# Kernel optimization log

Measured on AMD Instinct MI355X. Metric: run time of the kernel, lower is better.

The kernel has to match this reference:

```python
import jax, jax.numpy as jnp
import numpy as np

B, T, I, U = 64, 1024, 512, 1024


def ternary_quantize(w):
    # alpha = mean|w|; threshold = 0.7*alpha; map to {-alpha, 0, alpha}
    alpha = jnp.mean(jnp.abs(w))
    thr = 0.7 * alpha
    w_t = jnp.where(jnp.abs(w) < thr, jnp.zeros_like(w), jnp.sign(w))
    return alpha * w_t


def setup_inputs() -> dict:
    key = jax.random.key(0)
    k1, k2, k3 = jax.random.split(key, 3)
    x = jax.random.normal(k1, (B, T, I), dtype=jnp.float32)
    kernel = jax.random.normal(k2, (I, 4 * U), dtype=jnp.float32) * 0.05
    recurrent_kernel = jax.random.normal(k3, (U, 4 * U), dtype=jnp.float32) * 0.05
    # keras unit_forget_bias: zeros except ones on the forget-gate quarter
    bias = jnp.concatenate([jnp.zeros((U,)), jnp.ones((U,)), jnp.zeros((2 * U,))]).astype(jnp.float32)
    return {"x": x, "kernel": kernel, "recurrent_kernel": recurrent_kernel, "bias": bias}


def reference(x, kernel, recurrent_kernel, bias):
    kq = ternary_quantize(kernel)            # [I, 4U]
    rq = ternary_quantize(recurrent_kernel)  # [U, 4U]
    # Precompute input projection for all timesteps (math identical to per-step matmul)
    xz = jnp.einsum('bti,ig->btg', x, kq) + bias  # [B, T, 4U]
    xz_t = jnp.transpose(xz, (1, 0, 2))           # [T, B, 4U]

    def step(carry, zx):
        h, c = carry
        z = zx + h @ rq                            # [B, 4U]
        zi, zf, zg, zo = jnp.split(z, 4, axis=-1)  # keras gate order i, f, c, o
        i = jax.nn.sigmoid(zi)
        f = jax.nn.sigmoid(zf)
        g = jnp.tanh(zg)
        o = jax.nn.sigmoid(zo)
        c_new = f * c + i * g
        h_new = o * jnp.tanh(c_new)
        return (h_new, c_new), h_new

    h0 = jnp.zeros((x.shape[0], U), dtype=x.dtype)
    c0 = jnp.zeros((x.shape[0], U), dtype=x.dtype)
    _, hs = jax.lax.scan(step, (h0, c0), xz_t)     # hs: [T, B, U]
    return jnp.transpose(hs, (1, 0, 2))            # return_sequences=True -> [B, T, U]
```

## Files before the change

kernel.cpp:

```cpp
#include <hip/hip_runtime.h>
#include <hip/hip_bf16.h>


typedef __attribute__((ext_vector_type(8))) __bf16 bf16x8;
typedef __attribute__((ext_vector_type(4))) float f32x4;
typedef __attribute__((ext_vector_type(2))) unsigned int u32x2;

#define NWG 256
#define WGT 512
#define T_N 1024

__global__ void absum_kernel(const float* __restrict__ w, int n,
                             double* __restrict__ partial) {
  __shared__ double sd[256];
  double s = 0.0;
  for (int i = blockIdx.x * 256 + threadIdx.x; i < n; i += 256 * 256)
    s += fabs((double)w[i]);
  sd[threadIdx.x] = s;
  __syncthreads();
  for (int k = 128; k > 0; k >>= 1) {
    if (threadIdx.x < k) sd[threadIdx.x] += sd[threadIdx.x + k];
    __syncthreads();
  }
  if (threadIdx.x == 0) partial[blockIdx.x] = sd[0];
}

__global__ void alpha_finalize(const double* __restrict__ pk,
                               const double* __restrict__ pr,
                               float* __restrict__ alphas) {
  __shared__ double sd[256];
  int t = threadIdx.x;
  sd[t] = pk[t];
  __syncthreads();
  for (int s = 128; s > 0; s >>= 1) {
    if (t < s) sd[t] += sd[t + s];
    __syncthreads();
  }
  if (t == 0) alphas[0] = (float)(sd[0] / (512.0 * 4096.0));
  __syncthreads();
  sd[t] = pr[t];
  __syncthreads();
  for (int s = 128; s > 0; s >>= 1) {
    if (t < s) sd[t] += sd[t + s];
    __syncthreads();
  }
  if (t == 0) alphas[1] = (float)(sd[0] / (1024.0 * 4096.0));
}

__global__ void quant_kernel(const float* __restrict__ w, int kbits,
                             const float* __restrict__ alphas, int ai,
                             __hip_bfloat16* __restrict__ wt, int total) {
  int idx = blockIdx.x * 256 + threadIdx.x;
  if (idx >= total) return;
  float thr = 0.7f * alphas[ai];
  int K = 1 << kbits;
  int c = idx >> kbits;
  int k = idx & (K - 1);
  float v = w[k * 4096 + (c & 3) * 1024 + (c >> 2)];
  float q = (fabsf(v) < thr) ? 0.0f : ((v > 0.0f) ? 1.0f : ((v < 0.0f) ? -1.0f : 0.0f));
  wt[idx] = __float2bfloat16(q);
}

__device__ __forceinline__ bf16x8 cvt2(f32x4 a, f32x4 b) {
  bf16x8 r;
  r[0] = (__bf16)a[0]; r[1] = (__bf16)a[1];
  r[2] = (__bf16)a[2]; r[3] = (__bf16)a[3];
  r[4] = (__bf16)b[0]; r[5] = (__bf16)b[1];
  r[6] = (__bf16)b[2]; r[7] = (__bf16)b[3];
  return r;
}
__device__ __forceinline__ void ld16cc(bf16x8* d, const __hip_bfloat16* p) {
  asm volatile("global_load_dwordx4 %0, %1, off sc0 sc1"
               : "=v"(*d) : "v"(p) : "memory");
}
__device__ __forceinline__ void st8cc(__hip_bfloat16* p, u32x2 v) {
  asm volatile("global_store_dwordx2 %0, %1, off sc0 sc1" ::"v"(p), "v"(v)
               : "memory");
}
__device__ __forceinline__ void stflag(int* p, int v) {
  asm volatile("global_store_dword %0, %1, off sc0 sc1" ::"v"(p), "v"(v)
               : "memory");
}
__device__ __forceinline__ int ldflag(const int* p) {
  int v;
  asm volatile("global_load_dword %0, %1, off sc0 sc1\n\ts_waitcnt vmcnt(0)"
               : "=v"(v) : "v"(p) : "memory");
  return v;
}
__device__ __forceinline__ unsigned bf16b(float f) {
  return (unsigned)__builtin_bit_cast(unsigned short, __float2bfloat16(f));
}
__device__ __forceinline__ float sigm(float z) { return 1.0f / (1.0f + __expf(-z)); }
__device__ __forceinline__ float tanhx(float z) {
  float e = __expf(-2.0f * fabsf(z));
  return __builtin_copysignf((1.0f - e) / (1.0f + e), z);
}

__device__ __forceinline__ void wg_wait(const int* fl, int tgt, int* lflag,
                                        int lane, int wave) {
  if (wave == 7) {
    const int* p = fl + (lane & 31);
    for (;;) {
      int v = ldflag(p);
      if (__all(v >= tgt)) break;
      __builtin_amdgcn_s_sleep(1);
    }
    if (lane == 0)
      __hip_atomic_store(lflag, tgt, __ATOMIC_RELEASE,
                         __HIP_MEMORY_SCOPE_WORKGROUP);
  }
  while (__hip_atomic_load(lflag, __ATOMIC_ACQUIRE,
                           __HIP_MEMORY_SCOPE_WORKGROUP) < tgt) {}
}

__global__ void __launch_bounds__(WGT, 2)
lstm_persist(const float* __restrict__ bias4, const float* __restrict__ alphas,
             const float* __restrict__ x,
             const __hip_bfloat16* __restrict__ wtk,
             const __hip_bfloat16* __restrict__ wtr,
             __hip_bfloat16* __restrict__ hbuf,
             float* __restrict__ out,
             int* __restrict__ gctr) {
  extern __shared__ char lds[];
  char* lwtk = lds;
  float* lz = (float*)(lds + 131072);
  float* lxz = (float*)(lds + 147968);
  unsigned short* lhs = (unsigned short*)(lds + 156416);
  int* lmeta = (int*)(lds + 156928);

  const int tid = threadIdx.x;
  const int wg = blockIdx.x;
  const int lane = tid & 63;
  const int wave = tid >> 6;
  const int r16 = lane & 15;
  const int kb8 = (lane >> 4) << 3;

  const int g = wg >> 5;
  const int u = wg & 31;
  const int rb0 = g << 3;
  int* flagsg = gctr + 64 + g * 32;

  if (tid == 0) lmeta[0] = 0;

  for (int it = tid; it < 8192; it += WGT) {
    int c = it >> 6, kk = (it & 63) << 3;
    bf16x8 v = *(const bf16x8*)(wtk + (size_t)(u * 128 + c) * 512 + kk);
    *(bf16x8*)(lwtk + (c << 10) + ((kk << 1) ^ ((c & 7) << 4))) = v;
  }

  const int ks0 = (wave & 3) << 8;
  bf16x8 bw[8][4];
  {
    const __hip_bfloat16* wb =
        wtr + (size_t)(u * 128 + ((wave >> 2) << 6) + r16) * 1024 + ks0 + kb8;
#pragma unroll
    for (int ks = 0; ks < 8; ++ks)
#pragma unroll
      for (int nt = 0; nt < 4; ++nt)
        bw[ks][nt] = *(const bf16x8*)(wb + (size_t)nt * 16 * 1024 + (ks << 5));
  }

  const float ak = alphas[0];
  const float ar = alphas[1];

  const int rl = tid >> 5;
  const int ul = tid & 31;
  float bias_c[4];
#pragma unroll
  for (int gg = 0; gg < 4; ++gg)
    bias_c[gg] = bias4[gg * 1024 + u * 32 + ul];
  float cst = 0.0f;
  float* outp = out + ((size_t)(rb0 + rl) << 20) + u * 32 + ul;

  auto xproj = [&](int tt, int par) {
    const float* xr =
        x + ((size_t)(rb0 + (r16 & 7)) << 19) + ((size_t)tt << 9) + kb8;
    const int cloc = (wave << 4) + r16;
    const char* bbase = lwtk + (cloc << 10);
    const int bxor = (cloc & 7) << 4;
    f32x4 a = {0.f, 0.f, 0.f, 0.f};
#pragma unroll
    for (int kw = 0; kw < 16; ++kw) {
      bf16x8 af = cvt2(*(const f32x4*)(xr + kw * 32),
                       *(const f32x4*)(xr + kw * 32 + 4));
      bf16x8 bf = *(const bf16x8*)(bbase + ((((kw << 5) + kb8) << 1) ^ bxor));
      a = __builtin_amdgcn_mfma_f32_16x16x32_bf16(af, bf, a, 0, 0, 0);
    }
    if (lane < 32) {
      float* dst = lxz + par * 1056 + (wave << 4) + (lane & 15);
#pragma unroll
      for (int j = 0; j < 4; ++j)
        dst[(((lane >> 4) << 2) + j) * 132] = a[j];
    }
  };

  __syncthreads();
  xproj(0, 0);

  for (int t = 0; t < T_N; ++t) {
    {
      f32x4 acc[4];
#pragma unroll
      for (int nt = 0; nt < 4; ++nt) acc[nt] = (f32x4){0.f, 0.f, 0.f, 0.f};
      if (t > 0) {
        bf16x8 fr[8];
        if (r16 < 8) {
          const __hip_bfloat16* hrow =
              hbuf + ((t & 1) << 16) + (g << 13) + (r16 << 10) + ks0 + kb8;
#pragma unroll
          for (int ks = 0; ks < 8; ++ks) ld16cc(&fr[ks], hrow + (ks << 5));
        } else {
#pragma unroll
          for (int ks = 0; ks < 8; ++ks)
#pragma unroll
            for (int j = 0; j < 8; ++j) fr[ks][j] = (__bf16)0.0f;
        }
        asm volatile("s_waitcnt vmcnt(0)" ::: "memory");
        __builtin_amdgcn_sched_barrier(0);
#pragma unroll
        for (int ks = 0; ks < 8; ++ks)
#pragma unroll
          for (int nt = 0; nt < 4; ++nt)
            acc[nt] = __builtin_amdgcn_mfma_f32_16x16x32_bf16(
                fr[ks], bw[ks][nt], acc[nt], 0, 0, 0);
      }
      if (lane < 32) {
        float* dst = lz + (wave & 3) * 1056 + ((wave >> 2) << 6) + (lane & 15);
#pragma unroll
        for (int nt = 0; nt < 4; ++nt)
#pragma unroll
          for (int j = 0; j < 4; ++j)
            dst[(((lane >> 4) << 2) + j) * 132 + (nt << 4)] = acc[nt][j];
      }
    }
    __syncthreads();

    float ho = 0.0f;
    if (tid < 256) {
      f32x4 z0 = *(const f32x4*)(lz + 0 * 1056 + rl * 132 + (ul << 2));
      f32x4 z1 = *(const f32x4*)(lz + 1 * 1056 + rl * 132 + (ul << 2));
      f32x4 z2 = *(const f32x4*)(lz + 2 * 1056 + rl * 132 + (ul << 2));
      f32x4 z3 = *(const f32x4*)(lz + 3 * 1056 + rl * 132 + (ul << 2));
      f32x4 z = z0 + z1 + z2 + z3;
      f32x4 xv = *(const f32x4*)(lxz + (t & 1) * 1056 + rl * 132 + (ul << 2));
      float zi = ak * xv[0] + bias_c[0] + ar * z[0];
      float zf = ak * xv[1] + bias_c[1] + ar * z[1];
      float zg = ak * xv[2] + bias_c[2] + ar * z[2];
      float zo = ak * xv[3] + bias_c[3] + ar * z[3];
      float ig = sigm(zi), fg = sigm(zf), gg = tanhx(zg), og = sigm(zo);
      float cn = fg * cst + ig * gg;
      cst = cn;
      ho = og * tanhx(cn);
      lhs[tid] = (unsigned short)bf16b(ho);
    }
    __syncthreads();

    if (wave == 4) {
      u32x2 dv = *(const u32x2*)(lhs + (lane << 2));
      __hip_bfloat16* hb = hbuf + (((t + 1) & 1) << 16) + (g << 13) +
                           ((lane >> 3) << 10) + u * 32 + ((lane & 7) << 2);
      st8cc(hb, dv);
      asm volatile("s_waitcnt vmcnt(0)" ::: "memory");
      if (lane == 0) stflag(flagsg + u, t + 1);
    }

    if (tid < 256) outp[(size_t)t << 10] = ho;
    if (t != T_N - 1) xproj(t + 1, (t + 1) & 1);

    wg_wait(flagsg, t + 1, lmeta, lane, wave);
  }
}

extern "C" void kernel_launch(void* const* d_in, const int* in_sizes, int n_in,
                              void* d_out, int out_size, void* d_ws, size_t ws_size,
                              hipStream_t stream) {
  const float* x = (const float*)d_in[0];
  const float* wk = (const float*)d_in[1];
  const float* wr = (const float*)d_in[2];
  const float* bs = (const float*)d_in[3];
  float* out = (float*)d_out;
  char* ws = (char*)d_ws;

  float* alphas = (float*)(ws + 0);
  int* sync = (int*)(ws + 256);
  double* pk = (double*)(ws + 4096);
  double* pr = (double*)(ws + 6144);
  __hip_bfloat16* wtk = (__hip_bfloat16*)(ws + 8192);
  __hip_bfloat16* wtr = (__hip_bfloat16*)(ws + 8192 + (4 << 20));
  __hip_bfloat16* hbuf = (__hip_bfloat16*)(ws + 8192 + (12 << 20));

  absum_kernel<<<256, 256, 0, stream>>>(wk, 512 * 4096, pk);
  absum_kernel<<<256, 256, 0, stream>>>(wr, 1024 * 4096, pr);
  alpha_finalize<<<1, 256, 0, stream>>>(pk, pr, alphas);
  quant_kernel<<<(4096 * 512) / 256, 256, 0, stream>>>(wk, 9, alphas, 0, wtk,
                                                       4096 * 512);
  quant_kernel<<<(4096 * 1024) / 256, 256, 0, stream>>>(wr, 10, alphas, 1, wtr,
                                                        4096 * 1024);
  (void)hipMemsetAsync(sync, 0, 2048);

  const int smem = 131072 + 16896 + 8448 + 512 + 32;
  (void)hipFuncSetAttribute((const void*)lstm_persist,
                            hipFuncAttributeMaxDynamicSharedMemorySize, smem);
  void* args[] = {(void*)&bs,  (void*)&alphas, (void*)&x,   (void*)&wtk,
                  (void*)&wtr, (void*)&hbuf,   (void*)&out, (void*)&sync};
  (void)hipLaunchCooperativeKernel((void*)lstm_persist, dim3(NWG), dim3(WGT),
                                   args, smem, stream);
}
```

Before: 10.80 ms.

## Split per-step flag waits by K-slice and defer polling to next step

Replaces the end-of-step workgroup-wide wait on all 32 peer flags with a per-wave wait at the start of the next recurrent step. Each of waves 0-3 polls only the 8 producer flags covering its own K-slice of h, and waves 4-7 follow via LDS. This lets the next input-projection overlap with peers finishing. h is now stored directly per thread as 2-byte stores, dropping the LDS staging buffer and one barrier, and flags are regrouped by K-slice. The costs are more, smaller global stores per step and busy polling without sleep, which adds memory traffic.

```diff
diff --git a/kernel.cpp b/kernel.cpp
--- a/kernel.cpp
+++ b/kernel.cpp
@@ -4,7 +4,6 @@
 
 typedef __attribute__((ext_vector_type(8))) __bf16 bf16x8;
 typedef __attribute__((ext_vector_type(4))) float f32x4;
-typedef __attribute__((ext_vector_type(2))) unsigned int u32x2;
 
 #define NWG 256
 #define WGT 512
@@ -73,8 +72,8 @@
   asm volatile("global_load_dwordx4 %0, %1, off sc0 sc1"
                : "=v"(*d) : "v"(p) : "memory");
 }
-__device__ __forceinline__ void st8cc(__hip_bfloat16* p, u32x2 v) {
-  asm volatile("global_store_dwordx2 %0, %1, off sc0 sc1" ::"v"(p), "v"(v)
+__device__ __forceinline__ void st_cc2(__hip_bfloat16* p, unsigned bits) {
+  asm volatile("global_store_short %0, %1, off sc0 sc1" ::"v"(p), "v"(bits)
                : "memory");
 }
 __device__ __forceinline__ void stflag(int* p, int v) {
@@ -94,23 +93,6 @@
 __device__ __forceinline__ float tanhx(float z) {
   float e = __expf(-2.0f * fabsf(z));
   return __builtin_copysignf((1.0f - e) / (1.0f + e), z);
-}
-
-__device__ __forceinline__ void wg_wait(const int* fl, int tgt, int* lflag,
-                                        int lane, int wave) {
-  if (wave == 7) {
-    const int* p = fl + (lane & 31);
-    for (;;) {
-      int v = ldflag(p);
-      if (__all(v >= tgt)) break;
-      __builtin_amdgcn_s_sleep(1);
-    }
-    if (lane == 0)
-      __hip_atomic_store(lflag, tgt, __ATOMIC_RELEASE,
-                         __HIP_MEMORY_SCOPE_WORKGROUP);
-  }
-  while (__hip_atomic_load(lflag, __ATOMIC_ACQUIRE,
-                           __HIP_MEMORY_SCOPE_WORKGROUP) < tgt) {}
 }
 
 __global__ void __launch_bounds__(WGT, 2)
@@ -120,13 +102,12 @@
              const __hip_bfloat16* __restrict__ wtr,
              __hip_bfloat16* __restrict__ hbuf,
              float* __restrict__ out,
-             int* __restrict__ gctr) {
+             int* __restrict__ flags) {
   extern __shared__ char lds[];
   char* lwtk = lds;
   float* lz = (float*)(lds + 131072);
   float* lxz = (float*)(lds + 147968);
-  unsigned short* lhs = (unsigned short*)(lds + 156416);
-  int* lmeta = (int*)(lds + 156928);
+  int* lmeta = (int*)(lds + 156416);
 
   const int tid = threadIdx.x;
   const int wg = blockIdx.x;
@@ -138,9 +119,11 @@
   const int g = wg >> 5;
   const int u = wg & 31;
   const int rb0 = g << 3;
-  int* flagsg = gctr + 64 + g * 32;
-
-  if (tid == 0) lmeta[0] = 0;
+
+  if (tid < 4) lmeta[tid] = 0;
+
+  int* myflag = flags + ((g << 2) + (u >> 3)) * 32 + (u & 7);
+  const int* pollp = flags + ((g << 2) + (wave & 3)) * 32 + (lane & 7);
 
   for (int it = tid; it < 8192; it += WGT) {
     int c = it >> 6, kk = (it & 63) << 3;
@@ -170,6 +153,7 @@
   for (int gg = 0; gg < 4; ++gg)
     bias_c[gg] = bias4[gg * 1024 + u * 32 + ul];
   float cst = 0.0f;
+  __hip_bfloat16* hst = hbuf + (g << 13) + (rl << 10) + u * 32 + ul;
   float* outp = out + ((size_t)(rb0 + rl) << 20) + u * 32 + ul;
 
   auto xproj = [&](int tt, int par) {
@@ -203,6 +187,18 @@
 #pragma unroll
       for (int nt = 0; nt < 4; ++nt) acc[nt] = (f32x4){0.f, 0.f, 0.f, 0.f};
       if (t > 0) {
+        if (wave < 4) {
+          for (;;) {
+            int v = (lane < 8) ? ldflag(pollp) : 0x7fffffff;
+            if (__all(v >= t)) break;
+          }
+          if (lane == 0)
+            __hip_atomic_store(&lmeta[wave], t, __ATOMIC_RELEASE,
+                               __HIP_MEMORY_SCOPE_WORKGROUP);
+        } else {
+          while (__hip_atomic_load(&lmeta[wave - 4], __ATOMIC_ACQUIRE,
+                                   __HIP_MEMORY_SCOPE_WORKGROUP) < t) {}
+        }
         bf16x8 fr[8];
         if (r16 < 8) {
           const __hip_bfloat16* hrow =
@@ -251,23 +247,15 @@
       float cn = fg * cst + ig * gg;
       cst = cn;
       ho = og * tanhx(cn);
-      lhs[tid] = (unsigned short)bf16b(ho);
-    }
-    __syncthreads();
-
-    if (wave == 4) {
-      u32x2 dv = *(const u32x2*)(lhs + (lane << 2));
-      __hip_bfloat16* hb = hbuf + (((t + 1) & 1) << 16) + (g << 13) +
-                           ((lane >> 3) << 10) + u * 32 + ((lane & 7) << 2);
-      st8cc(hb, dv);
+      st_cc2(hst + (((t + 1) & 1) << 16), bf16b(ho));
       asm volatile("s_waitcnt vmcnt(0)" ::: "memory");
-      if (lane == 0) stflag(flagsg + u, t + 1);
-    }
+    }
+    __syncthreads();
+
+    if (wave == 4 && lane == 0) stflag(myflag, t + 1);
 
     if (tid < 256) outp[(size_t)t << 10] = ho;
     if (t != T_N - 1) xproj(t + 1, (t + 1) & 1);
-
-    wg_wait(flagsg, t + 1, lmeta, lane, wave);
   }
 }
 
@@ -282,12 +270,12 @@
   char* ws = (char*)d_ws;
 
   float* alphas = (float*)(ws + 0);
-  int* sync = (int*)(ws + 256);
-  double* pk = (double*)(ws + 4096);
-  double* pr = (double*)(ws + 6144);
-  __hip_bfloat16* wtk = (__hip_bfloat16*)(ws + 8192);
-  __hip_bfloat16* wtr = (__hip_bfloat16*)(ws + 8192 + (4 << 20));
-  __hip_bfloat16* hbuf = (__hip_bfloat16*)(ws + 8192 + (12 << 20));
+  double* pk = (double*)(ws + 1024);
+  int* flags = (int*)(ws + 4096);
+  double* pr = (double*)(ws + 8192);
+  __hip_bfloat16* wtk = (__hip_bfloat16*)(ws + 16384);
+  __hip_bfloat16* wtr = (__hip_bfloat16*)(ws + 16384 + (4 << 20));
+  __hip_bfloat16* hbuf = (__hip_bfloat16*)(ws + 16384 + (12 << 20));
 
   absum_kernel<<<256, 256, 0, stream>>>(wk, 512 * 4096, pk);
   absum_kernel<<<256, 256, 0, stream>>>(wr, 1024 * 4096, pr);
@@ -296,13 +284,13 @@
                                                        4096 * 512);
   quant_kernel<<<(4096 * 1024) / 256, 256, 0, stream>>>(wr, 10, alphas, 1, wtr,
                                                         4096 * 1024);
-  (void)hipMemsetAsync(sync, 0, 2048);
-
-  const int smem = 131072 + 16896 + 8448 + 512 + 32;
+  (void)hipMemsetAsync(flags, 0, 4096);
+
+  const int smem = 131072 + 16896 + 8448 + 64;
   (void)hipFuncSetAttribute((const void*)lstm_persist,
                             hipFuncAttributeMaxDynamicSharedMemorySize, smem);
   void* args[] = {(void*)&bs,  (void*)&alphas, (void*)&x,   (void*)&wtk,
-                  (void*)&wtr, (void*)&hbuf,   (void*)&out, (void*)&sync};
+                  (void*)&wtr, (void*)&hbuf,   (void*)&out, (void*)&flags};
   (void)hipLaunchCooperativeKernel((void*)lstm_persist, dim3(NWG), dim3(WGT),
                                    args, smem, stream);
 }
```

Result: slower. 11.14 ms, median of 2 (+3.2%).
